# Kernel tuning notes

Measured on AMD Instinct MI355X. Metric: run time of the kernel, lower is better.

The kernel has to match this reference:

```python
import jax, jax.numpy as jnp
import numpy as np

N_TOKENS = 16384  # bs*slen = 4*4096
HIDDEN = 2048
EXPERTS = 8
TOPK = 2
EPS = 1e-20


def setup_inputs() -> dict:
    key = jax.random.key(0)
    k1, k2, k3 = jax.random.split(key, 3)
    x = jax.random.normal(k1, (N_TOKENS, HIDDEN), dtype=jnp.float32)
    W = jax.random.normal(k2, (EXPERTS, HIDDEN), dtype=jnp.float32) * 0.02
    expert_bias = jax.random.normal(k3, (EXPERTS,), dtype=jnp.float32) * 0.01
    return {"x": x, "W": W, "expert_bias": expert_bias}


def reference(x, W, expert_bias):
    # gate: linear without bias -> (N, experts)
    logits = jnp.einsum("nd,ed->ne", x, W)
    scores = jax.nn.sigmoid(logits.astype(jnp.float32))
    # topk on biased scores, but gather unbiased scores
    _, selected_experts_indices = jax.lax.top_k(scores + expert_bias[None, :], TOPK)
    top_scores = jnp.take_along_axis(scores, selected_experts_indices, axis=1)
    # renormalize
    top_scores = top_scores / (top_scores.sum(axis=-1, keepdims=True) + EPS)
    # entropy on detached scores
    d = jax.lax.stop_gradient(top_scores)
    experts_entropy = -(d * jnp.log(d)).sum(axis=-1).mean()
    # histogram over expert indices (torch.histc with bins=E, min=0, max=E)
    num_tokens_per_expert = jnp.bincount(
        selected_experts_indices.reshape(-1), length=EXPERTS
    )
    return (top_scores, scores, selected_experts_indices,
            num_tokens_per_expert, experts_entropy)
```

## Files before the change

kernel.cpp:

```cpp
#include <hip/hip_runtime.h>
#include <math.h>

#define NT  16384
#define HID 2048
#define NE  8
#define NBLK 512

constexpr int TOP_OFF  = 0;
constexpr int SC_OFF   = NT * 2;
constexpr int IDX_OFF  = SC_OFF + NT * NE;
constexpr int HIST_OFF = IDX_OFF + NT * 2;
constexpr int ENT_OFF  = HIST_OFF + NE;

constexpr int WS_ROW = 12;

typedef float f32x4 __attribute__((ext_vector_type(4)));

static __device__ __forceinline__ f32x4 ntload4(const float* p) {
  return __builtin_nontemporal_load(reinterpret_cast<const f32x4*>(p));
}

__global__ void init_tail(float* __restrict__ out) {
  const int i = threadIdx.x;
  if (i < NE + 1) out[HIST_OFF + i] = 0.0f;
}

#define FOR_E(F) F(0) F(1) F(2) F(3) F(4) F(5) F(6) F(7)

template <bool USE_WS>
__global__ __launch_bounds__(512, 4)
void router_kernel(const float* __restrict__ x, const float* __restrict__ W,
                   const float* __restrict__ bias, float* __restrict__ out,
                   float* __restrict__ ws) {
  __shared__ float sW[NE * HID];
  __shared__ int   sHist[NE];
  __shared__ float sEnt;

  const int tid  = threadIdx.x;
  const int wave = tid >> 6;
  const int lane = tid & 63;

  const int t0 = blockIdx.x * 32 + wave * 4;
  const float* xb = x + (size_t)t0 * HID;
  const int phase = (wave + (int)blockIdx.x) & 7;

#define OFFX(it) ((((it) + phase) & 7) * 256 + lane * 4)
#define XLOAD(N, off)                                                      \
  N##0 = ntload4(xb + (off));                                              \
  N##1 = ntload4(xb + HID + (off));                                        \
  N##2 = ntload4(xb + 2 * HID + (off));                                    \
  N##3 = ntload4(xb + 3 * HID + (off));

  f32x4 A0, A1, A2, A3, B0, B1, B2, B3;

  { const int o0 = OFFX(0); XLOAD(A, o0) }

#if __has_builtin(__builtin_amdgcn_global_load_lds)
  {
    const float4* Wv  = reinterpret_cast<const float4*>(W);
    float4*       sWv = reinterpret_cast<float4*>(sW);
#pragma unroll
    for (int i = 0; i < 8; ++i) {
      const float4* gsrc = Wv + i * 512 + tid;
      float4*       ldst = sWv + i * 512 + wave * 64;
      __builtin_amdgcn_global_load_lds(
          (const __attribute__((address_space(1))) void*)gsrc,
          (__attribute__((address_space(3))) void*)ldst, 16, 0, 0);
    }
  }
#else
  {
    const float4* Wv  = reinterpret_cast<const float4*>(W);
    float4*       sWv = reinterpret_cast<float4*>(sW);
#pragma unroll
    for (int i = 0; i < 8; ++i) sWv[i * 512 + tid] = Wv[i * 512 + tid];
  }
#endif
  if (tid < NE) sHist[tid] = 0;
  if (tid == 0) sEnt = 0.0f;

#define DECL_BS(e) const float bs_##e = bias[e];
  FOR_E(DECL_BS)

  __syncthreads();

#define DECL_ACC(e) float a0_##e = 0.f, a1_##e = 0.f, a2_##e = 0.f, a3_##e = 0.f;
  FOR_E(DECL_ACC)

#define FMA_E(e, q0, q1, q2, q3, offc)                                     \
  {                                                                        \
    const float4 wv = *reinterpret_cast<const float4*>(sW + e * HID + (offc)); \
    a0_##e += q0.x * wv.x + q0.y * wv.y + q0.z * wv.z + q0.w * wv.w;       \
    a1_##e += q1.x * wv.x + q1.y * wv.y + q1.z * wv.z + q1.w * wv.w;       \
    a2_##e += q2.x * wv.x + q2.y * wv.y + q2.z * wv.z + q2.w * wv.w;       \
    a3_##e += q3.x * wv.x + q3.y * wv.y + q3.z * wv.z + q3.w * wv.w;       \
  }

#define FMA_ALL(q0, q1, q2, q3, offc)                                      \
    FMA_E(0, q0, q1, q2, q3, offc) FMA_E(1, q0, q1, q2, q3, offc)          \
    FMA_E(2, q0, q1, q2, q3, offc) FMA_E(3, q0, q1, q2, q3, offc)          \
    FMA_E(4, q0, q1, q2, q3, offc) FMA_E(5, q0, q1, q2, q3, offc)          \
    FMA_E(6, q0, q1, q2, q3, offc) FMA_E(7, q0, q1, q2, q3, offc)

#define BODY(C, N, itc)                                                    \
  {                                                                        \
    const int offn = OFFX(itc + 1);                                        \
    XLOAD(N, offn)                                                         \
    const f32x4 q0 = C##0 , q1 = C##1 , q2 = C##2 , q3 = C##3 ;            \
    const int offc = OFFX(itc);                                            \
    FMA_ALL(q0, q1, q2, q3, offc)                                          \
  }
#define BODY_LAST(C, itc)                                                  \
  {                                                                        \
    const f32x4 q0 = C##0 , q1 = C##1 , q2 = C##2 , q3 = C##3 ;            \
    const int offc = OFFX(itc);                                            \
    FMA_ALL(q0, q1, q2, q3, offc)                                          \
  }

  BODY(A, B, 0)
  BODY(B, A, 1)
  BODY(A, B, 2)
  BODY(B, A, 3)
  BODY(A, B, 4)
  BODY(B, A, 5)
  BODY(A, B, 6)
  BODY_LAST(B, 7)

  const bool lo  = (lane < 32);
  const bool md  = ((lane & 16) == 0);
#define STAGE_A(e)                                                         \
  float b0_##e, b1_##e;                                                    \
  {                                                                        \
    float s0 = lo ? a2_##e : a0_##e;                                       \
    float s1 = lo ? a3_##e : a1_##e;                                       \
    const float r0 = __shfl_xor(s0, 32, 64);                               \
    const float r1 = __shfl_xor(s1, 32, 64);                               \
    b0_##e = (lo ? a0_##e : a2_##e) + r0;                                  \
    b1_##e = (lo ? a1_##e : a3_##e) + r1;                                  \
  }
  FOR_E(STAGE_A)
#define STAGE_B(e)                                                         \
  float c_##e;                                                             \
  {                                                                        \
    float s = md ? b1_##e : b0_##e;                                        \
    const float r = __shfl_xor(s, 16, 64);                                 \
    c_##e = (md ? b0_##e : b1_##e) + r;                                    \
  }
  FOR_E(STAGE_B)
#define STAGE_CF(e)                                                        \
  c_##e += __shfl_xor(c_##e, 8, 64);                                       \
  c_##e += __shfl_xor(c_##e, 4, 64);                                       \
  c_##e += __shfl_xor(c_##e, 2, 64);                                       \
  c_##e += __shfl_xor(c_##e, 1, 64);
  FOR_E(STAGE_CF)

  const int tok = t0 + (lane >> 4);
#define SIG_E(e) const float sc_##e = 1.0f / (1.0f + __expf(-c_##e));
  FOR_E(SIG_E)

  float m1 = -1e30f, m2 = -1e30f, s1 = 0.0f, s2 = 0.0f;
  int i1 = 0, i2 = 0;
#define TOP_E(e)                                                           \
  {                                                                        \
    const float be = sc_##e + bs_##e;                                      \
    const bool g1 = be > m1;                                               \
    const bool g2 = be > m2;                                               \
    i2 = g1 ? i1 : (g2 ? e     : i2);                                      \
    m2 = g1 ? m1 : (g2 ? be    : m2);                                      \
    s2 = g1 ? s1 : (g2 ? sc_##e : s2);                                     \
    i1 = g1 ? e     : i1;                                                  \
    m1 = g1 ? be    : m1;                                                  \
    s1 = g1 ? sc_##e : s1;                                                 \
  }
  FOR_E(TOP_E)

  const float denom = s1 + s2 + 1e-20f;
  const float n1 = s1 / denom;
  const float n2 = s2 / denom;
  float ent = -(n1 * __logf(n1) + n2 * __logf(n2));
  float ent2 = ent + __shfl_xor(ent, 16, 64);
  float ent4 = ent2 + __shfl_xor(ent2, 32, 64);

  if ((lane & 15) == 0) {
    *reinterpret_cast<float2*>(out + TOP_OFF + (size_t)tok * 2) =
        make_float2(n1, n2);
    *reinterpret_cast<float2*>(out + IDX_OFF + (size_t)tok * 2) =
        make_float2((float)i1, (float)i2);
    *reinterpret_cast<float4*>(out + SC_OFF + (size_t)tok * 8) =
        make_float4(sc_0, sc_1, sc_2, sc_3);
    *reinterpret_cast<float4*>(out + SC_OFF + (size_t)tok * 8 + 4) =
        make_float4(sc_4, sc_5, sc_6, sc_7);
    atomicAdd(&sHist[i1], 1);
    atomicAdd(&sHist[i2], 1);
  }
  if (lane == 0) atomicAdd(&sEnt, ent4);

  __syncthreads();
  if (USE_WS) {
    if (tid < NE) ws[(size_t)blockIdx.x * WS_ROW + tid] = (float)sHist[tid];
    if (tid == NE) ws[(size_t)blockIdx.x * WS_ROW + NE] = sEnt;
  } else {
    if (tid < NE) atomicAdd(out + HIST_OFF + tid, (float)sHist[tid]);
    if (tid == 0) atomicAdd(out + ENT_OFF, sEnt * (1.0f / (float)NT));
  }
}

__global__ __launch_bounds__(512)
void finalize(const float* __restrict__ ws, float* __restrict__ out) {
  __shared__ float red[8][9];
  const int tid  = threadIdx.x;
  const int wave = tid >> 6;
  const int lane = tid & 63;

  const float4* p = reinterpret_cast<const float4*>(ws + (size_t)tid * WS_ROW);
  const float4 v0 = p[0];
  const float4 v1 = p[1];
  const float4 v2 = p[2];
  float h0 = v0.x, h1 = v0.y, h2 = v0.z, h3 = v0.w;
  float h4 = v1.x, h5 = v1.y, h6 = v1.z, h7 = v1.w, ent = v2.x;

#define REDF(v)                                                            \
  { v += __shfl_xor(v, 32, 64); v += __shfl_xor(v, 16, 64);                \
    v += __shfl_xor(v,  8, 64); v += __shfl_xor(v,  4, 64);                \
    v += __shfl_xor(v,  2, 64); v += __shfl_xor(v,  1, 64); }
  REDF(h0) REDF(h1) REDF(h2) REDF(h3) REDF(h4) REDF(h5) REDF(h6) REDF(h7)
  REDF(ent)

  if (lane == 0) {
    red[wave][0] = h0; red[wave][1] = h1; red[wave][2] = h2; red[wave][3] = h3;
    red[wave][4] = h4; red[wave][5] = h5; red[wave][6] = h6; red[wave][7] = h7;
    red[wave][8] = ent;
  }
  __syncthreads();
  if (tid < NE + 1) {
    float s = 0.f;
#pragma unroll
    for (int w = 0; w < 8; ++w) s += red[w][tid];
    if (tid < NE) out[HIST_OFF + tid] = s;
    else          out[ENT_OFF] = s * (1.0f / (float)NT);
  }
}

extern "C" void kernel_launch(void* const* d_in, const int* in_sizes, int n_in,
                              void* d_out, int out_size, void* d_ws, size_t ws_size,
                              hipStream_t stream) {
  (void)in_sizes; (void)n_in; (void)out_size;
  const float* x    = (const float*)d_in[0];
  const float* W    = (const float*)d_in[1];
  const float* bias = (const float*)d_in[2];
  float* out = (float*)d_out;

  const bool use_ws = (d_ws != nullptr) &&
                      (ws_size >= (size_t)NBLK * WS_ROW * sizeof(float));
  if (use_ws) {
    router_kernel<true><<<NBLK, 512, 0, stream>>>(x, W, bias, out, (float*)d_ws);
    finalize<<<1, 512, 0, stream>>>((const float*)d_ws, out);
  } else {
    init_tail<<<1, 64, 0, stream>>>(out);
    router_kernel<false><<<NBLK, 512, 0, stream>>>(x, W, bias, out, (float*)d_ws);
  }
}
```

Baseline: 30.31 us.

## Fuse finalize into router kernel via last-block atomic counter

Removes the separate finalize kernel launch. Each block writes its partial histogram and entropy to the workspace, fences, and bumps a global counter. The block that sees the last count runs the reduction in place. This saves one launch and the gap between kernels, but adds a fence and atomic to every block plus a serialized tail reduction. The counter is never reset and relies on wraparound modulo NBLK across calls.

```diff
diff --git a/kernel.cpp b/kernel.cpp
--- a/kernel.cpp
+++ b/kernel.cpp
@@ -12,7 +12,8 @@
 constexpr int HIST_OFF = IDX_OFF + NT * 2;
 constexpr int ENT_OFF  = HIST_OFF + NE;
 
-constexpr int WS_ROW = 12;
+constexpr int WS_ROW  = 12;
+constexpr int CNT_OFF = NBLK * WS_ROW;
 
 typedef float f32x4 __attribute__((ext_vector_type(4)));
 
@@ -27,7 +28,43 @@
 
 #define FOR_E(F) F(0) F(1) F(2) F(3) F(4) F(5) F(6) F(7)
 
-template <bool USE_WS>
+__device__ __forceinline__ void finalize_body(const float* __restrict__ ws,
+                                              float* __restrict__ out) {
+  __shared__ float red[8][9];
+  const int tid  = threadIdx.x;
+  const int wave = tid >> 6;
+  const int lane = tid & 63;
+
+  const float4* p = reinterpret_cast<const float4*>(ws + (size_t)tid * WS_ROW);
+  const float4 v0 = p[0];
+  const float4 v1 = p[1];
+  const float4 v2 = p[2];
+  float h0 = v0.x, h1 = v0.y, h2 = v0.z, h3 = v0.w;
+  float h4 = v1.x, h5 = v1.y, h6 = v1.z, h7 = v1.w, ent = v2.x;
+
+#define REDF(v)                                                            \
+  { v += __shfl_xor(v, 32, 64); v += __shfl_xor(v, 16, 64);                \
+    v += __shfl_xor(v,  8, 64); v += __shfl_xor(v,  4, 64);                \
+    v += __shfl_xor(v,  2, 64); v += __shfl_xor(v,  1, 64); }
+  REDF(h0) REDF(h1) REDF(h2) REDF(h3) REDF(h4) REDF(h5) REDF(h6) REDF(h7)
+  REDF(ent)
+
+  if (lane == 0) {
+    red[wave][0] = h0; red[wave][1] = h1; red[wave][2] = h2; red[wave][3] = h3;
+    red[wave][4] = h4; red[wave][5] = h5; red[wave][6] = h6; red[wave][7] = h7;
+    red[wave][8] = ent;
+  }
+  __syncthreads();
+  if (tid < NE + 1) {
+    float s = 0.f;
+#pragma unroll
+    for (int w = 0; w < 8; ++w) s += red[w][tid];
+    if (tid < NE) out[HIST_OFF + tid] = s;
+    else          out[ENT_OFF] = s * (1.0f / (float)NT);
+  }
+}
+
+template <bool LASTBLK>
 __global__ __launch_bounds__(512, 4)
 void router_kernel(const float* __restrict__ x, const float* __restrict__ W,
                    const float* __restrict__ bias, float* __restrict__ out,
@@ -35,6 +72,7 @@
   __shared__ float sW[NE * HID];
   __shared__ int   sHist[NE];
   __shared__ float sEnt;
+  __shared__ int   sLast;
 
   const int tid  = threadIdx.x;
   const int wave = tid >> 6;
@@ -196,48 +234,24 @@
   if (lane == 0) atomicAdd(&sEnt, ent4);
 
   __syncthreads();
-  if (USE_WS) {
+  if (LASTBLK) {
     if (tid < NE) ws[(size_t)blockIdx.x * WS_ROW + tid] = (float)sHist[tid];
     if (tid == NE) ws[(size_t)blockIdx.x * WS_ROW + NE] = sEnt;
+    __syncthreads();
+    if (tid == 0) {
+      __threadfence();
+      const unsigned old =
+          atomicAdd(reinterpret_cast<unsigned*>(ws + CNT_OFF), 1u);
+      sLast = ((old & (NBLK - 1)) == (NBLK - 1)) ? 1 : 0;
+    }
+    __syncthreads();
+    if (sLast) {
+      __threadfence();
+      finalize_body(ws, out);
+    }
   } else {
     if (tid < NE) atomicAdd(out + HIST_OFF + tid, (float)sHist[tid]);
     if (tid == 0) atomicAdd(out + ENT_OFF, sEnt * (1.0f / (float)NT));
-  }
-}
-
-__global__ __launch_bounds__(512)
-void finalize(const float* __restrict__ ws, float* __restrict__ out) {
-  __shared__ float red[8][9];
-  const int tid  = threadIdx.x;
-  const int wave = tid >> 6;
-  const int lane = tid & 63;
-
-  const float4* p = reinterpret_cast<const float4*>(ws + (size_t)tid * WS_ROW);
-  const float4 v0 = p[0];
-  const float4 v1 = p[1];
-  const float4 v2 = p[2];
-  float h0 = v0.x, h1 = v0.y, h2 = v0.z, h3 = v0.w;
-  float h4 = v1.x, h5 = v1.y, h6 = v1.z, h7 = v1.w, ent = v2.x;
-
-#define REDF(v)                                                            \
-  { v += __shfl_xor(v, 32, 64); v += __shfl_xor(v, 16, 64);                \
-    v += __shfl_xor(v,  8, 64); v += __shfl_xor(v,  4, 64);                \
-    v += __shfl_xor(v,  2, 64); v += __shfl_xor(v,  1, 64); }
-  REDF(h0) REDF(h1) REDF(h2) REDF(h3) REDF(h4) REDF(h5) REDF(h6) REDF(h7)
-  REDF(ent)
-
-  if (lane == 0) {
-    red[wave][0] = h0; red[wave][1] = h1; red[wave][2] = h2; red[wave][3] = h3;
-    red[wave][4] = h4; red[wave][5] = h5; red[wave][6] = h6; red[wave][7] = h7;
-    red[wave][8] = ent;
-  }
-  __syncthreads();
-  if (tid < NE + 1) {
-    float s = 0.f;
-#pragma unroll
-    for (int w = 0; w < 8; ++w) s += red[w][tid];
-    if (tid < NE) out[HIST_OFF + tid] = s;
-    else          out[ENT_OFF] = s * (1.0f / (float)NT);
   }
 }
 
@@ -249,14 +263,14 @@
   const float* W    = (const float*)d_in[1];
   const float* bias = (const float*)d_in[2];
   float* out = (float*)d_out;
+  float* wsf = (float*)d_ws;
 
   const bool use_ws = (d_ws != nullptr) &&
-                      (ws_size >= (size_t)NBLK * WS_ROW * sizeof(float));
+                      (ws_size >= (size_t)(CNT_OFF + 4) * sizeof(float));
   if (use_ws) {
-    router_kernel<true><<<NBLK, 512, 0, stream>>>(x, W, bias, out, (float*)d_ws);
-    finalize<<<1, 512, 0, stream>>>((const float*)d_ws, out);
+    router_kernel<true><<<NBLK, 512, 0, stream>>>(x, W, bias, out, wsf);
   } else {
     init_tail<<<1, 64, 0, stream>>>(out);
-    router_kernel<false><<<NBLK, 512, 0, stream>>>(x, W, bias, out, (float*)d_ws);
-  }
-}
+    router_kernel<false><<<NBLK, 512, 0, stream>>>(x, W, bias, out, wsf);
+  }
+}
```

After: 48.61 us. 1.6x slower.
